# Performance work log

Measured on AMD Instinct MI355X. Metric: run time of the kernel, lower is better.

Reference implementation:

```python
import jax, jax.numpy as jnp
import numpy as np

BLK = 128          # quantization block size (group_shape = (1,128) act, (128,128) weight)
FP8_MAX = 448.0    # max finite value of float8_e4m3fn
EPS = 1e-6         # RMSNorm epsilon


def _rms_norm(x, weight):
    # RMSNorm: x / sqrt(mean(x^2) + eps) * weight
    var = jnp.mean(x * x, axis=-1, keepdims=True)
    return x * jax.lax.rsqrt(var + EPS) * weight


def _quant_dequant_act(x):
    # Per-token-group (1, BLK) dynamic FP8 quantization, then dequant (fake-quant).
    M, K = x.shape
    g = x.reshape(M, K // BLK, BLK)
    scale = jnp.maximum(jnp.max(jnp.abs(g), axis=-1, keepdims=True) / FP8_MAX, 1e-10)
    q = jnp.clip(g / scale, -FP8_MAX, FP8_MAX)
    q = q.astype(jnp.float8_e4m3fn).astype(jnp.float32)
    return (q * scale).reshape(M, K)


def _dequant_weight(w_fp8, ws):
    # w_fp8: [N, K] fp8-rounded values in fp32; ws: [N//BLK, K//BLK] block scales.
    s_full = jnp.repeat(jnp.repeat(ws, BLK, axis=0), BLK, axis=1)  # [N, K]
    return w_fp8 * s_full


def setup_inputs() -> dict:
    key = jax.random.key(0)
    k1, k2, k3, k4 = jax.random.split(key, 4)
    T, H = 4096, 4096
    x = jax.random.normal(k1, (T, H), dtype=jnp.float32)
    norm_w = jax.random.uniform(k2, (4, H), dtype=jnp.float32)
    w = jax.random.uniform(k3, (3, H, H), dtype=jnp.float32)
    wscale = jax.random.uniform(k4, (3, H // BLK, H // BLK), dtype=jnp.float32)
    return {"x": x, "norm_w": norm_w, "w": w, "wscale": wscale}


def reference(x, norm_w, w, wscale):
    # Weights are stored as FP8 in the original model (torch.rand(...).to(FP8_DTYPE)).
    w_fp8 = w.astype(jnp.float8_e4m3fn).astype(jnp.float32)  # [3, H, H]

    x = jax.nn.relu(x)
    resid = x
    # norm[0]: plain RMSNorm
    y = _rms_norm(x, norm_w[0])
    for i in range(3):
        # block-FP8 linear: quantize activation, dequantize weight, out = a @ W^T
        a = _quant_dequant_act(y)                    # [T, H]
        wd = _dequant_weight(w_fp8[i], wscale[i])    # [H, H]
        xi = a @ wd.T                                # [T, H]
        # fused add + RMSNorm: resid = xi + resid; y = rmsnorm(resid)
        resid = xi + resid
        y = _rms_norm(resid, norm_w[i + 1])
    return y
```

## Files before the change

kernel.cpp:

```cpp
#include <hip/hip_runtime.h>

typedef float f32x4 __attribute__((ext_vector_type(4)));
typedef int i32x4 __attribute__((ext_vector_type(4)));
typedef int i32x8 __attribute__((ext_vector_type(8)));

#define HDIM 4096
#define NKB 32

__global__ __launch_bounds__(256) void wquant_kernel(const float* __restrict__ w,
                                                     unsigned char* __restrict__ w8,
                                                     int n4) {
  int i = blockIdx.x * 256 + threadIdx.x;
  if (i >= n4) return;
  const float4 v = ((const float4*)w)[i];
  int p = 0;
  p = __builtin_amdgcn_cvt_pk_fp8_f32(v.x, v.y, p, false);
  p = __builtin_amdgcn_cvt_pk_fp8_f32(v.z, v.w, p, true);
  ((int*)w8)[i] = p;
}

template <int MODE>
__global__ __launch_bounds__(256) void norm_quant_kernel(
    const float* __restrict__ src, float* __restrict__ resid,
    const float* __restrict__ nw, unsigned char* __restrict__ qa,
    float* __restrict__ ascT, float* __restrict__ out) {
  const int row = blockIdx.x;
  const int tid = threadIdx.x;
  const float* srow = src + (size_t)row * HDIM;
  float4 v[4];
  float ss = 0.f;
#pragma unroll
  for (int c = 0; c < 4; ++c) {
    float4 t = ((const float4*)srow)[c * 256 + tid];
    if (MODE == 0) {
      t.x = fmaxf(t.x, 0.f); t.y = fmaxf(t.y, 0.f);
      t.z = fmaxf(t.z, 0.f); t.w = fmaxf(t.w, 0.f);
      ((float4*)(resid + (size_t)row * HDIM))[c * 256 + tid] = t;
    }
    v[c] = t;
    ss += t.x * t.x + t.y * t.y + t.z * t.z + t.w * t.w;
  }
#pragma unroll
  for (int m = 32; m >= 1; m >>= 1) ss += __shfl_xor(ss, m);
  __shared__ float red[4];
  if ((tid & 63) == 0) red[tid >> 6] = ss;
  __syncthreads();
  const float tot = red[0] + red[1] + red[2] + red[3];
  const float rstd = rsqrtf(tot * (1.f / (float)HDIM) + 1e-6f);
#pragma unroll
  for (int c = 0; c < 4; ++c) {
    float4 wv = ((const float4*)nw)[c * 256 + tid];
    float4 y;
    y.x = v[c].x * rstd * wv.x;
    y.y = v[c].y * rstd * wv.y;
    y.z = v[c].z * rstd * wv.z;
    y.w = v[c].w * rstd * wv.w;
    if (MODE == 2) {
      ((float4*)(out + (size_t)row * HDIM))[c * 256 + tid] = y;
    } else {
      float amax = fmaxf(fmaxf(fabsf(y.x), fabsf(y.y)), fmaxf(fabsf(y.z), fabsf(y.w)));
#pragma unroll
      for (int m = 16; m >= 1; m >>= 1) amax = fmaxf(amax, __shfl_xor(amax, m));
      const float scale = fmaxf(amax / 448.f, 1e-10f);
      const float qinv = __builtin_amdgcn_rcpf(scale);
      float qx = fminf(fmaxf(y.x * qinv, -448.f), 448.f);
      float qy = fminf(fmaxf(y.y * qinv, -448.f), 448.f);
      float qz = fminf(fmaxf(y.z * qinv, -448.f), 448.f);
      float qw = fminf(fmaxf(y.w * qinv, -448.f), 448.f);
      int p = 0;
      p = __builtin_amdgcn_cvt_pk_fp8_f32(qx, qy, p, false);
      p = __builtin_amdgcn_cvt_pk_fp8_f32(qz, qw, p, true);
      const int off = (c * 256 + tid) << 2;
      *(int*)(qa + (size_t)row * HDIM + off) = p;
      if ((tid & 31) == 0) ascT[(c * 8 + (tid >> 5)) * HDIM + row] = scale;
    }
  }
}

__global__ __launch_bounds__(512, 2) void gemm256_kernel(
    const unsigned char* __restrict__ qa, const float* __restrict__ ascT,
    const unsigned char* __restrict__ w8, const float* __restrict__ wsc,
    float* __restrict__ resid) {
  extern __shared__ char smem[];
  char* ldsA = smem;
  char* ldsB = smem + 65536;
  char* ldsS = smem + 131072;

  const int tid = threadIdx.x;
  const int lane = tid & 63;
  const int wid = tid >> 6;
  const int wm = wid >> 1;
  const int wn = wid & 1;

  const int bflat = blockIdx.y * 16 + blockIdx.x;
  const int bswz = (bflat & 7) * 32 + (bflat >> 3);
  const int m0 = (bswz >> 4) << 8;
  const int n0 = (bswz & 15) << 8;

  const int ln15 = lane & 15;
  const int g = lane >> 4;

  int ofs[4];
  {
    const int rowp = ((tid >> 7) & 3) * 16 + (tid & 15);
    const int kp = ((tid >> 4) & 3) * 32 + ((tid >> 6) & 1) * 16;
#pragma unroll
    for (int ch = 0; ch < 4; ++ch) ofs[ch] = (ch * 64 + rowp) * HDIM + kp;
  }
  const unsigned char* gA = qa + (size_t)m0 * HDIM;
  const unsigned char* gB = w8 + (size_t)n0 * HDIM;
  const float* sS = ascT + m0 + lane * 4;

  const int nb = __builtin_amdgcn_readfirstlane((n0 >> 7) + wn);
  const float* wsp = wsc + nb * NKB;

  const int abase = wm * 8192 + lane * 16;
  const int bbase = wn * 16384 + lane * 16;
  const int svb = wm * 256 + g * 16;

  f32x4 acc[4][8];
#pragma unroll
  for (int i = 0; i < 4; ++i)
#pragma unroll
    for (int j = 0; j < 8; ++j) acc[i][j] = (f32x4){0.f, 0.f, 0.f, 0.f};

  i32x8 aF[4];
  i32x8 bFa[2];
  i32x8 bFb[2];
  f32x4 svw[4];

#define STAGE_A(CH, KB, BUF)                                                              \
  __builtin_amdgcn_global_load_lds(                                                       \
      (const __attribute__((address_space(1))) void*)(gA + ofs[CH] + (KB)*128),           \
      (__attribute__((address_space(3))) void*)(ldsA + (BUF)*32768 + (CH)*8192 + tid*16), \
      16, 0, 0)
#define STAGE_B(CH, KB, BUF)                                                              \
  __builtin_amdgcn_global_load_lds(                                                       \
      (const __attribute__((address_space(1))) void*)(gB + ofs[CH] + (KB)*128),           \
      (__attribute__((address_space(3))) void*)(ldsB + (BUF)*32768 + (CH)*8192 + tid*16), \
      16, 0, 0)
#define STAGE_S(KB, BUF)                                                                  \
  __builtin_amdgcn_global_load_lds(                                                       \
      (const __attribute__((address_space(1))) void*)(sS + (size_t)(KB)*HDIM),            \
      (__attribute__((address_space(3))) void*)(ldsS + (BUF)*1024 + lane*16), 16, 0, 0)

#define RD_A(MT)                                                                          \
  {                                                                                       \
    const char* pA_ = ldsA + cb + abase + (MT)*2048;                                      \
    i32x4 lo_ = *(const i32x4*)pA_;                                                       \
    i32x4 hi_ = *(const i32x4*)(pA_ + 1024);                                              \
    aF[MT] = __builtin_shufflevector(lo_, hi_, 0, 1, 2, 3, 4, 5, 6, 7);                   \
  }
#define RD_SVW(MT) svw[MT] = *(const f32x4*)(ldsS + cur * 1024 + svb + (MT)*64) * sw;
#define RD_BS(BS, NH)                                                                     \
  {                                                                                       \
    const char* p0_ = ldsB + cb + bbase + ((NH)*2) * 2048;                                \
    i32x4 l0_ = *(const i32x4*)p0_;                                                       \
    i32x4 h0_ = *(const i32x4*)(p0_ + 1024);                                              \
    BS[0] = __builtin_shufflevector(l0_, h0_, 0, 1, 2, 3, 4, 5, 6, 7);                    \
    const char* p1_ = p0_ + 2048;                                                         \
    i32x4 l1_ = *(const i32x4*)p1_;                                                       \
    i32x4 h1_ = *(const i32x4*)(p1_ + 1024);                                              \
    BS[1] = __builtin_shufflevector(l1_, h1_, 0, 1, 2, 3, 4, 5, 6, 7);                    \
  }

#define PH_WAIT                                                                           \
  asm volatile("s_waitcnt lgkmcnt(0)" ::: "memory");                                      \
  __builtin_amdgcn_sched_barrier(0);

#define MFMA_PH(MTA, MTB, NH, BS)                                                         \
  __builtin_amdgcn_s_setprio(1);                                                          \
  {                                                                                       \
    const f32x4 z_ = (f32x4){0.f, 0.f, 0.f, 0.f};                                         \
    f32x4 t0 = __builtin_amdgcn_mfma_scale_f32_16x16x128_f8f6f4(                          \
        aF[MTA], BS[0], z_, 0, 0, 0, 127, 0, 127);                                        \
    f32x4 t1 = __builtin_amdgcn_mfma_scale_f32_16x16x128_f8f6f4(                          \
        aF[MTA], BS[1], z_, 0, 0, 0, 127, 0, 127);                                        \
    f32x4 t2 = __builtin_amdgcn_mfma_scale_f32_16x16x128_f8f6f4(                          \
        aF[MTB], BS[0], z_, 0, 0, 0, 127, 0, 127);                                        \
    f32x4 t3 = __builtin_amdgcn_mfma_scale_f32_16x16x128_f8f6f4(                          \
        aF[MTB], BS[1], z_, 0, 0, 0, 127, 0, 127);                                        \
    __builtin_amdgcn_s_setprio(0);                                                        \
    acc[MTA][(NH)*2]     += t0 * svw[MTA];                                                \
    acc[MTA][(NH)*2 + 1] += t1 * svw[MTA];                                                \
    acc[MTB][(NH)*2]     += t2 * svw[MTB];                                                \
    acc[MTB][(NH)*2 + 1] += t3 * svw[MTB];                                                \
  }

  STAGE_S(0, 0); STAGE_A(0, 0, 0); STAGE_A(1, 0, 0); STAGE_A(2, 0, 0); STAGE_A(3, 0, 0);
  STAGE_B(0, 0, 0); STAGE_B(2, 0, 0); STAGE_B(1, 0, 0); STAGE_B(3, 0, 0);
  asm volatile("s_waitcnt vmcnt(0)" ::: "memory");
  __builtin_amdgcn_s_barrier();
  __builtin_amdgcn_sched_barrier(0);

#pragma unroll 2
  for (int kb = 0; kb < NKB; ++kb) {
    const int cur = kb & 1;
    const int nxt = cur ^ 1;
    const int kbn = (kb + 1) & (NKB - 1);
    const int cb = cur * 32768;
    const float sw = wsp[kb];
    RD_A(0) RD_A(1) RD_SVW(0) RD_SVW(1) RD_BS(bFa, 0)
    STAGE_S(kbn, nxt); STAGE_A(0, kbn, nxt);
    PH_WAIT MFMA_PH(0, 1, 0, bFa)
    RD_A(2) RD_A(3) RD_SVW(2) RD_SVW(3)
    STAGE_A(1, kbn, nxt); STAGE_A(2, kbn, nxt);
    PH_WAIT MFMA_PH(2, 3, 0, bFa)
    RD_BS(bFb, 1)
    STAGE_A(3, kbn, nxt); STAGE_B(0, kbn, nxt); STAGE_B(2, kbn, nxt);
    PH_WAIT MFMA_PH(2, 3, 1, bFb)
    STAGE_B(1, kbn, nxt); STAGE_B(3, kbn, nxt);
    PH_WAIT MFMA_PH(0, 1, 1, bFb)
    RD_BS(bFa, 2)
    PH_WAIT MFMA_PH(0, 1, 2, bFa)
    PH_WAIT MFMA_PH(2, 3, 2, bFa)
    RD_BS(bFb, 3)
    PH_WAIT MFMA_PH(2, 3, 3, bFb)
    PH_WAIT MFMA_PH(0, 1, 3, bFb)
    asm volatile("s_waitcnt vmcnt(0)" ::: "memory");
    __builtin_amdgcn_s_barrier();
    __builtin_amdgcn_sched_barrier(0);
  }

  const size_t rowstart = (size_t)(m0 + wm * 64 + g * 4) * HDIM + n0 + wn * 128 + ln15;
#pragma unroll
  for (int mt = 0; mt < 4; ++mt)
#pragma unroll
    for (int ntg = 0; ntg < 8; ++ntg)
#pragma unroll
      for (int j = 0; j < 4; ++j) {
        const size_t idx = rowstart + (size_t)(mt * 16 + j) * HDIM + ntg * 16;
        resid[idx] += acc[mt][ntg][j];
      }
#undef MFMA_PH
#undef PH_WAIT
#undef RD_BS
#undef RD_SVW
#undef RD_A
#undef STAGE_A
#undef STAGE_B
#undef STAGE_S
}

extern "C" void kernel_launch(void* const* d_in, const int* in_sizes, int n_in,
                              void* d_out, int out_size, void* d_ws, size_t ws_size,
                              hipStream_t stream) {
  const float* x = (const float*)d_in[0];
  const float* norm_w = (const float*)d_in[1];
  const float* w = (const float*)d_in[2];
  const float* wscale = (const float*)d_in[3];
  float* out = (float*)d_out;
  char* ws = (char*)d_ws;

  size_t off = 0;
  unsigned char* w8 = (unsigned char*)(ws + off); off += 3ull * HDIM * HDIM;
  float* resid = (float*)(ws + off);              off += (size_t)HDIM * HDIM * 4;
  unsigned char* qa = (unsigned char*)(ws + off); off += (size_t)HDIM * HDIM;
  float* asc = (float*)(ws + off);                off += (size_t)NKB * HDIM * 4;

  hipFuncSetAttribute((const void*)gemm256_kernel,
                      hipFuncAttributeMaxDynamicSharedMemorySize, 133120);

  const int n4 = 3 * HDIM * HDIM / 4;
  wquant_kernel<<<n4 / 256, 256, 0, stream>>>(w, w8, n4);
  norm_quant_kernel<0><<<HDIM, 256, 0, stream>>>(x, resid, norm_w, qa, asc, nullptr);
  for (int i = 0; i < 3; ++i) {
    gemm256_kernel<<<dim3(16, 16), 512, 133120, stream>>>(
        qa, asc, w8 + (size_t)i * HDIM * HDIM, wscale + i * NKB * NKB, resid);
    if (i < 2)
      norm_quant_kernel<1><<<HDIM, 256, 0, stream>>>(resid, nullptr, norm_w + (size_t)(i + 1) * HDIM, qa, asc, nullptr);
    else
      norm_quant_kernel<2><<<HDIM, 256, 0, stream>>>(resid, nullptr, norm_w + (size_t)3 * HDIM, nullptr, nullptr, out);
  }
}
```

Baseline: 442.7 us.

## Shrink GEMM tile from 256x256 to 128x128 to raise occupancy

Reduces the block tile of the block-scaled FP8 GEMM from 256x256 to 128x128. The grid grows from 256 to 1024 blocks, LDS use per block halves, and launch bounds now allow 4 blocks per CU. The per-iteration MFMA schedule is simplified to two phases. The intent is better CU utilisation and more latency hiding, at the cost of lower arithmetic intensity and twice the global and LDS traffic per FLOP.

```diff
diff --git a/kernel.cpp b/kernel.cpp
--- a/kernel.cpp
+++ b/kernel.cpp
@@ -77,14 +77,14 @@
   }
 }
 
-__global__ __launch_bounds__(512, 2) void gemm256_kernel(
+__global__ __launch_bounds__(512, 4) void gemm256_kernel(
     const unsigned char* __restrict__ qa, const float* __restrict__ ascT,
     const unsigned char* __restrict__ w8, const float* __restrict__ wsc,
     float* __restrict__ resid) {
   extern __shared__ char smem[];
   char* ldsA = smem;
-  char* ldsB = smem + 65536;
-  char* ldsS = smem + 131072;
+  char* ldsB = smem + 32768;
+  char* ldsS = smem + 65536;
 
   const int tid = threadIdx.x;
   const int lane = tid & 63;
@@ -92,54 +92,54 @@
   const int wm = wid >> 1;
   const int wn = wid & 1;
 
-  const int bflat = blockIdx.y * 16 + blockIdx.x;
-  const int bswz = (bflat & 7) * 32 + (bflat >> 3);
-  const int m0 = (bswz >> 4) << 8;
-  const int n0 = (bswz & 15) << 8;
+  const int bflat = blockIdx.y * 32 + blockIdx.x;
+  const int bswz = (bflat & 7) * 128 + (bflat >> 3);
+  const int m0 = (bswz >> 5) << 7;
+  const int n0 = (bswz & 31) << 7;
 
   const int ln15 = lane & 15;
   const int g = lane >> 4;
 
-  int ofs[4];
+  int ofs[2];
   {
     const int rowp = ((tid >> 7) & 3) * 16 + (tid & 15);
     const int kp = ((tid >> 4) & 3) * 32 + ((tid >> 6) & 1) * 16;
 #pragma unroll
-    for (int ch = 0; ch < 4; ++ch) ofs[ch] = (ch * 64 + rowp) * HDIM + kp;
+    for (int ch = 0; ch < 2; ++ch) ofs[ch] = (ch * 64 + rowp) * HDIM + kp;
   }
   const unsigned char* gA = qa + (size_t)m0 * HDIM;
   const unsigned char* gB = w8 + (size_t)n0 * HDIM;
   const float* sS = ascT + m0 + lane * 4;
 
-  const int nb = __builtin_amdgcn_readfirstlane((n0 >> 7) + wn);
-  const float* wsp = wsc + nb * NKB;
-
-  const int abase = wm * 8192 + lane * 16;
-  const int bbase = wn * 16384 + lane * 16;
-  const int svb = wm * 256 + g * 16;
-
-  f32x4 acc[4][8];
-#pragma unroll
-  for (int i = 0; i < 4; ++i)
-#pragma unroll
-    for (int j = 0; j < 8; ++j) acc[i][j] = (f32x4){0.f, 0.f, 0.f, 0.f};
-
-  i32x8 aF[4];
+  const float* wsp = wsc + (n0 >> 7) * NKB;
+
+  const int abase = wm * 4096 + lane * 16;
+  const int bbase = wn * 8192 + lane * 16;
+  const int svb = wm * 128 + g * 16;
+
+  f32x4 acc[2][4];
+#pragma unroll
+  for (int i = 0; i < 2; ++i)
+#pragma unroll
+    for (int j = 0; j < 4; ++j) acc[i][j] = (f32x4){0.f, 0.f, 0.f, 0.f};
+
+  i32x8 aF[2];
   i32x8 bFa[2];
   i32x8 bFb[2];
-  f32x4 svw[4];
+  f32x4 svw[2];
 
 #define STAGE_A(CH, KB, BUF)                                                              \
   __builtin_amdgcn_global_load_lds(                                                       \
       (const __attribute__((address_space(1))) void*)(gA + ofs[CH] + (KB)*128),           \
-      (__attribute__((address_space(3))) void*)(ldsA + (BUF)*32768 + (CH)*8192 + tid*16), \
+      (__attribute__((address_space(3))) void*)(ldsA + (BUF)*16384 + (CH)*8192 + tid*16), \
       16, 0, 0)
 #define STAGE_B(CH, KB, BUF)                                                              \
   __builtin_amdgcn_global_load_lds(                                                       \
       (const __attribute__((address_space(1))) void*)(gB + ofs[CH] + (KB)*128),           \
-      (__attribute__((address_space(3))) void*)(ldsB + (BUF)*32768 + (CH)*8192 + tid*16), \
+      (__attribute__((address_space(3))) void*)(ldsB + (BUF)*16384 + (CH)*8192 + tid*16), \
       16, 0, 0)
 #define STAGE_S(KB, BUF)                                                                  \
+  if (lane < 32)                                                                          \
   __builtin_amdgcn_global_load_lds(                                                       \
       (const __attribute__((address_space(1))) void*)(sS + (size_t)(KB)*HDIM),            \
       (__attribute__((address_space(3))) void*)(ldsS + (BUF)*1024 + lane*16), 16, 0, 0)
@@ -152,43 +152,39 @@
     aF[MT] = __builtin_shufflevector(lo_, hi_, 0, 1, 2, 3, 4, 5, 6, 7);                   \
   }
 #define RD_SVW(MT) svw[MT] = *(const f32x4*)(ldsS + cur * 1024 + svb + (MT)*64) * sw;
-#define RD_BS(BS, NH)                                                                     \
+#define RD_B(NT, DST)                                                                     \
   {                                                                                       \
-    const char* p0_ = ldsB + cb + bbase + ((NH)*2) * 2048;                                \
-    i32x4 l0_ = *(const i32x4*)p0_;                                                       \
-    i32x4 h0_ = *(const i32x4*)(p0_ + 1024);                                              \
-    BS[0] = __builtin_shufflevector(l0_, h0_, 0, 1, 2, 3, 4, 5, 6, 7);                    \
-    const char* p1_ = p0_ + 2048;                                                         \
-    i32x4 l1_ = *(const i32x4*)p1_;                                                       \
-    i32x4 h1_ = *(const i32x4*)(p1_ + 1024);                                              \
-    BS[1] = __builtin_shufflevector(l1_, h1_, 0, 1, 2, 3, 4, 5, 6, 7);                    \
+    const char* pB_ = ldsB + cb + bbase + (NT)*2048;                                      \
+    i32x4 lo_ = *(const i32x4*)pB_;                                                       \
+    i32x4 hi_ = *(const i32x4*)(pB_ + 1024);                                              \
+    DST = __builtin_shufflevector(lo_, hi_, 0, 1, 2, 3, 4, 5, 6, 7);                      \
   }
 
 #define PH_WAIT                                                                           \
   asm volatile("s_waitcnt lgkmcnt(0)" ::: "memory");                                      \
   __builtin_amdgcn_sched_barrier(0);
 
-#define MFMA_PH(MTA, MTB, NH, BS)                                                         \
+#define MFMA_PH(NH, BS)                                                                   \
   __builtin_amdgcn_s_setprio(1);                                                          \
   {                                                                                       \
     const f32x4 z_ = (f32x4){0.f, 0.f, 0.f, 0.f};                                         \
     f32x4 t0 = __builtin_amdgcn_mfma_scale_f32_16x16x128_f8f6f4(                          \
-        aF[MTA], BS[0], z_, 0, 0, 0, 127, 0, 127);                                        \
+        aF[0], BS[0], z_, 0, 0, 0, 127, 0, 127);                                          \
     f32x4 t1 = __builtin_amdgcn_mfma_scale_f32_16x16x128_f8f6f4(                          \
-        aF[MTA], BS[1], z_, 0, 0, 0, 127, 0, 127);                                        \
+        aF[0], BS[1], z_, 0, 0, 0, 127, 0, 127);                                          \
     f32x4 t2 = __builtin_amdgcn_mfma_scale_f32_16x16x128_f8f6f4(                          \
-        aF[MTB], BS[0], z_, 0, 0, 0, 127, 0, 127);                                        \
+        aF[1], BS[0], z_, 0, 0, 0, 127, 0, 127);                                          \
     f32x4 t3 = __builtin_amdgcn_mfma_scale_f32_16x16x128_f8f6f4(                          \
-        aF[MTB], BS[1], z_, 0, 0, 0, 127, 0, 127);                                        \
+        aF[1], BS[1], z_, 0, 0, 0, 127, 0, 127);                                          \
     __builtin_amdgcn_s_setprio(0);                                                        \
-    acc[MTA][(NH)*2]     += t0 * svw[MTA];                                                \
-    acc[MTA][(NH)*2 + 1] += t1 * svw[MTA];                                                \
-    acc[MTB][(NH)*2]     += t2 * svw[MTB];                                                \
-    acc[MTB][(NH)*2 + 1] += t3 * svw[MTB];                                                \
-  }
-
-  STAGE_S(0, 0); STAGE_A(0, 0, 0); STAGE_A(1, 0, 0); STAGE_A(2, 0, 0); STAGE_A(3, 0, 0);
-  STAGE_B(0, 0, 0); STAGE_B(2, 0, 0); STAGE_B(1, 0, 0); STAGE_B(3, 0, 0);
+    acc[0][(NH)*2]     += t0 * svw[0];                                                    \
+    acc[0][(NH)*2 + 1] += t1 * svw[0];                                                    \
+    acc[1][(NH)*2]     += t2 * svw[1];                                                    \
+    acc[1][(NH)*2 + 1] += t3 * svw[1];                                                    \
+  }
+
+  STAGE_S(0, 0);
+  STAGE_A(0, 0, 0); STAGE_A(1, 0, 0); STAGE_B(0, 0, 0); STAGE_B(1, 0, 0);
   asm volatile("s_waitcnt vmcnt(0)" ::: "memory");
   __builtin_amdgcn_s_barrier();
   __builtin_amdgcn_sched_barrier(0);
@@ -198,35 +194,25 @@
     const int cur = kb & 1;
     const int nxt = cur ^ 1;
     const int kbn = (kb + 1) & (NKB - 1);
-    const int cb = cur * 32768;
+    const int cb = cur * 16384;
     const float sw = wsp[kb];
-    RD_A(0) RD_A(1) RD_SVW(0) RD_SVW(1) RD_BS(bFa, 0)
-    STAGE_S(kbn, nxt); STAGE_A(0, kbn, nxt);
-    PH_WAIT MFMA_PH(0, 1, 0, bFa)
-    RD_A(2) RD_A(3) RD_SVW(2) RD_SVW(3)
-    STAGE_A(1, kbn, nxt); STAGE_A(2, kbn, nxt);
-    PH_WAIT MFMA_PH(2, 3, 0, bFa)
-    RD_BS(bFb, 1)
-    STAGE_A(3, kbn, nxt); STAGE_B(0, kbn, nxt); STAGE_B(2, kbn, nxt);
-    PH_WAIT MFMA_PH(2, 3, 1, bFb)
-    STAGE_B(1, kbn, nxt); STAGE_B(3, kbn, nxt);
-    PH_WAIT MFMA_PH(0, 1, 1, bFb)
-    RD_BS(bFa, 2)
-    PH_WAIT MFMA_PH(0, 1, 2, bFa)
-    PH_WAIT MFMA_PH(2, 3, 2, bFa)
-    RD_BS(bFb, 3)
-    PH_WAIT MFMA_PH(2, 3, 3, bFb)
-    PH_WAIT MFMA_PH(0, 1, 3, bFb)
+    RD_A(0) RD_A(1) RD_SVW(0) RD_SVW(1) RD_B(0, bFa[0]) RD_B(1, bFa[1])
+    STAGE_S(kbn, nxt);
+    STAGE_A(0, kbn, nxt); STAGE_A(1, kbn, nxt);
+    STAGE_B(0, kbn, nxt); STAGE_B(1, kbn, nxt);
+    PH_WAIT MFMA_PH(0, bFa)
+    RD_B(2, bFb[0]) RD_B(3, bFb[1])
+    PH_WAIT MFMA_PH(1, bFb)
     asm volatile("s_waitcnt vmcnt(0)" ::: "memory");
     __builtin_amdgcn_s_barrier();
     __builtin_amdgcn_sched_barrier(0);
   }
 
-  const size_t rowstart = (size_t)(m0 + wm * 64 + g * 4) * HDIM + n0 + wn * 128 + ln15;
-#pragma unroll
-  for (int mt = 0; mt < 4; ++mt)
-#pragma unroll
-    for (int ntg = 0; ntg < 8; ++ntg)
+  const size_t rowstart = (size_t)(m0 + wm * 32 + g * 4) * HDIM + n0 + wn * 64 + ln15;
+#pragma unroll
+  for (int mt = 0; mt < 2; ++mt)
+#pragma unroll
+    for (int ntg = 0; ntg < 4; ++ntg)
 #pragma unroll
       for (int j = 0; j < 4; ++j) {
         const size_t idx = rowstart + (size_t)(mt * 16 + j) * HDIM + ntg * 16;
@@ -234,7 +220,7 @@
       }
 #undef MFMA_PH
 #undef PH_WAIT
-#undef RD_BS
+#undef RD_B
 #undef RD_SVW
 #undef RD_A
 #undef STAGE_A
@@ -259,13 +245,13 @@
   float* asc = (float*)(ws + off);                off += (size_t)NKB * HDIM * 4;
 
   hipFuncSetAttribute((const void*)gemm256_kernel,
-                      hipFuncAttributeMaxDynamicSharedMemorySize, 133120);
+                      hipFuncAttributeMaxDynamicSharedMemorySize, 67584);
 
   const int n4 = 3 * HDIM * HDIM / 4;
   wquant_kernel<<<n4 / 256, 256, 0, stream>>>(w, w8, n4);
   norm_quant_kernel<0><<<HDIM, 256, 0, stream>>>(x, resid, norm_w, qa, asc, nullptr);
   for (int i = 0; i < 3; ++i) {
-    gemm256_kernel<<<dim3(16, 16), 512, 133120, stream>>>(
+    gemm256_kernel<<<dim3(32, 32), 512, 67584, stream>>>(
         qa, asc, w8 + (size_t)i * HDIM * HDIM, wscale + i * NKB * NKB, resid);
     if (i < 2)
       norm_quant_kernel<1><<<HDIM, 256, 0, stream>>>(resid, nullptr, norm_w + (size_t)(i + 1) * HDIM, qa, asc, nullptr);
```

Measured after the change: 1.186 ms. +168.0%, slower.
